# Performance work log

Hardware: AMD Instinct MI355X
Metric: run time of the kernel (lower is better)

## Reference

```python
import jax, jax.numpy as jnp
import numpy as np

NEG_SLOPE = 0.2       # PyG GATConv default leaky_relu negative_slope
NUM_GRAPHS = 128
VOCAB, HID, HEADS, NCLS = 5000, 64, 4, 20
N_NODES, N_EDGES = 50000, 1600000


def gat_conv(x, src, dst, W, a_src, a_dst, bias, concat):
    """PyG-style GATConv (eval mode, self-loops already in src/dst).
    W: [in, H*C]; a_src/a_dst: [H, C]; bias: [H*C] if concat else [C]."""
    N = x.shape[0]
    H, C = a_src.shape
    h = (x @ W).reshape(N, H, C)                      # [N,H,C]
    al_src = jnp.sum(h * a_src, axis=-1)              # [N,H]
    al_dst = jnp.sum(h * a_dst, axis=-1)              # [N,H]
    e = al_src[src] + al_dst[dst]                     # [E,H]
    e = jnp.where(e > 0, e, NEG_SLOPE * e)            # leaky_relu
    # segment softmax over incoming edges of each dst node
    emax = jax.lax.stop_gradient(jax.ops.segment_max(e, dst, num_segments=N))
    emax = jnp.where(jnp.isfinite(emax), emax, 0.0)
    ex = jnp.exp(e - emax[dst])
    denom = jax.ops.segment_sum(ex, dst, num_segments=N)
    alpha = ex / (denom[dst] + 1e-16)                 # [E,H]
    out = jax.ops.segment_sum(h[src] * alpha[..., None], dst, num_segments=N)  # [N,H,C]
    out = out.reshape(N, H * C) if concat else out.mean(axis=1)
    return out + bias


def setup_inputs() -> dict:
    key = jax.random.key(0)
    ks = jax.random.split(key, 12)
    C1 = HID // HEADS

    def xavier(k, shape):
        fan_in, fan_out = shape[0], shape[-1]
        lim = np.sqrt(6.0 / (fan_in + fan_out))
        return jax.random.uniform(k, shape, jnp.float32, -lim, lim)

    return {
        "x": jax.random.normal(ks[0], (N_NODES, VOCAB), jnp.float32),
        "edge_index": jax.random.randint(ks[1], (2, N_EDGES), 0, N_NODES, jnp.int32),
        "batch": jnp.sort(jax.random.randint(ks[2], (N_NODES,), 0, NUM_GRAPHS, jnp.int32)),
        "W1": xavier(ks[3], (VOCAB, HID)),
        "a_src1": xavier(ks[4], (HEADS, C1)),
        "a_dst1": xavier(ks[5], (HEADS, C1)),
        "b1": jnp.zeros((HID,), jnp.float32),
        "W2": xavier(ks[6], (HID, HID)),
        "a_src2": xavier(ks[7], (1, HID)),
        "a_dst2": xavier(ks[8], (1, HID)),
        "b2": jnp.zeros((HID,), jnp.float32),
        "Wc": xavier(ks[9], (HID, NCLS)),
        "bc": jnp.zeros((NCLS,), jnp.float32),
    }


def reference(x, edge_index, batch, W1, a_src1, a_dst1, b1,
              W2, a_src2, a_dst2, b2, Wc, bc):
    N = x.shape[0]
    loop = jnp.arange(N, dtype=edge_index.dtype)
    src = jnp.concatenate([edge_index[0], loop])      # add self-loops (PyG default)
    dst = jnp.concatenate([edge_index[1], loop])

    h = jax.nn.elu(gat_conv(x, src, dst, W1, a_src1, a_dst1, b1, concat=True))
    h = jax.nn.elu(gat_conv(h, src, dst, W2, a_src2, a_dst2, b2, concat=False))

    # global_mean_pool over batch ids
    sums = jax.ops.segment_sum(h, batch, num_segments=NUM_GRAPHS)           # [G,HID]
    cnts = jax.ops.segment_sum(jnp.ones((N, 1), h.dtype), batch, num_segments=NUM_GRAPHS)
    pooled = sums / jnp.maximum(cnts, 1.0)

    logits = pooled @ Wc + bc
    return jax.nn.log_softmax(logits, axis=1)
```

## Files before the change

### kernel.cpp

```cpp
#include <hip/hip_runtime.h>

#define N_NODES 50000
#define VOCAB   5000
#define KPAD1   5024
#define HID     64
#define HEADS   4
#define NCLS    20
#define NGRAPH  128
#define N_EDGES 1600000
#define ETOT    (N_EDGES + N_NODES)

typedef __attribute__((ext_vector_type(8))) short short8;
typedef __attribute__((ext_vector_type(4))) float f32x4;

__device__ inline ushort f2bf(float x) {
  union { float f; unsigned u; } c; c.f = x;
  unsigned r = (c.u + 0x7fffu + ((c.u >> 16) & 1u)) >> 16;
  return (ushort)r;
}

__global__ void cvtT_kernel(const float* __restrict__ W, ushort* __restrict__ Bt,
                            int K, int KP) {
  int i = blockIdx.x * blockDim.x + threadIdx.x;
  if (i >= 64 * KP) return;
  int n = i / KP, k = i - n * KP;
  Bt[i] = (k < K) ? f2bf(W[(size_t)k * 64 + n]) : (ushort)0;
}

template<int KT, int KP>
__global__ __launch_bounds__(256) void gemm_stream(const float* __restrict__ A,
    const ushort* __restrict__ Bt, float* __restrict__ D, int M) {
  int gt = blockIdx.x * 256 + threadIdx.x;
  int gw = gt >> 6, lane = gt & 63;
  int lr = lane & 15, quad = lane >> 4;
  int m0 = gw * 16;
  if (m0 >= M) return;
  const float*  ap = A  + (size_t)(m0 + lr) * KT + quad * 8;
  const ushort* bp = Bt + (size_t)lr * KP + quad * 8;
  f32x4 acc[4] = {{0,0,0,0},{0,0,0,0},{0,0,0,0},{0,0,0,0}};
  constexpr int KF = (KT / 32) * 32;
  #pragma unroll 2
  for (int k0 = 0; k0 < KF; k0 += 32) {
    float4 v0 = *(const float4*)(ap + k0);
    float4 v1 = *(const float4*)(ap + k0 + 4);
    short8 b0 = *(const short8*)(bp + k0);
    short8 b1 = *(const short8*)(bp + 16 * KP + k0);
    short8 b2 = *(const short8*)(bp + 32 * KP + k0);
    short8 b3 = *(const short8*)(bp + 48 * KP + k0);
    short8 af;
    af[0] = (short)f2bf(v0.x); af[1] = (short)f2bf(v0.y);
    af[2] = (short)f2bf(v0.z); af[3] = (short)f2bf(v0.w);
    af[4] = (short)f2bf(v1.x); af[5] = (short)f2bf(v1.y);
    af[6] = (short)f2bf(v1.z); af[7] = (short)f2bf(v1.w);
    acc[0] = __builtin_amdgcn_mfma_f32_16x16x32_bf16(af, b0, acc[0], 0, 0, 0);
    acc[1] = __builtin_amdgcn_mfma_f32_16x16x32_bf16(af, b1, acc[1], 0, 0, 0);
    acc[2] = __builtin_amdgcn_mfma_f32_16x16x32_bf16(af, b2, acc[2], 0, 0, 0);
    acc[3] = __builtin_amdgcn_mfma_f32_16x16x32_bf16(af, b3, acc[3], 0, 0, 0);
  }
  if (KT % 32) {
    int k0 = KF;
    float4 v0 = make_float4(0,0,0,0), v1 = make_float4(0,0,0,0);
    if (quad == 0) { v0 = *(const float4*)(ap + k0); v1 = *(const float4*)(ap + k0 + 4); }
    short8 b0 = *(const short8*)(bp + k0);
    short8 b1 = *(const short8*)(bp + 16 * KP + k0);
    short8 b2 = *(const short8*)(bp + 32 * KP + k0);
    short8 b3 = *(const short8*)(bp + 48 * KP + k0);
    short8 af;
    af[0] = (short)f2bf(v0.x); af[1] = (short)f2bf(v0.y);
    af[2] = (short)f2bf(v0.z); af[3] = (short)f2bf(v0.w);
    af[4] = (short)f2bf(v1.x); af[5] = (short)f2bf(v1.y);
    af[6] = (short)f2bf(v1.z); af[7] = (short)f2bf(v1.w);
    acc[0] = __builtin_amdgcn_mfma_f32_16x16x32_bf16(af, b0, acc[0], 0, 0, 0);
    acc[1] = __builtin_amdgcn_mfma_f32_16x16x32_bf16(af, b1, acc[1], 0, 0, 0);
    acc[2] = __builtin_amdgcn_mfma_f32_16x16x32_bf16(af, b2, acc[2], 0, 0, 0);
    acc[3] = __builtin_amdgcn_mfma_f32_16x16x32_bf16(af, b3, acc[3], 0, 0, 0);
  }
  #pragma unroll
  for (int ct = 0; ct < 4; ++ct)
    #pragma unroll
    for (int r = 0; r < 4; ++r)
      D[(size_t)(m0 + quad * 4 + r) * 64 + ct * 16 + lr] = acc[ct][r];
}

__global__ void al_h4_kernel(const float* __restrict__ h, const float* __restrict__ a_src,
                             const float* __restrict__ a_dst, float* __restrict__ alS,
                             float* __restrict__ alD, int n) {
  int wid = (blockIdx.x * blockDim.x + threadIdx.x) >> 6;
  int lane = threadIdx.x & 63;
  if (wid >= n) return;
  float hv = h[(size_t)wid * 64 + lane];
  float s = hv * a_src[lane];
  float d = hv * a_dst[lane];
  #pragma unroll
  for (int off = 1; off < 16; off <<= 1) {
    s += __shfl_down(s, off, 16);
    d += __shfl_down(d, off, 16);
  }
  if ((lane & 15) == 0) {
    alS[wid * 4 + (lane >> 4)] = s;
    alD[wid * 4 + (lane >> 4)] = d;
  }
}

__global__ void al_h1_kernel(const float* __restrict__ h, const float* __restrict__ a_src,
                             const float* __restrict__ a_dst, float* __restrict__ alS,
                             float* __restrict__ alD, int n) {
  int wid = (blockIdx.x * blockDim.x + threadIdx.x) >> 6;
  int lane = threadIdx.x & 63;
  if (wid >= n) return;
  float hv = h[(size_t)wid * 64 + lane];
  float s = hv * a_src[lane];
  float d = hv * a_dst[lane];
  #pragma unroll
  for (int off = 1; off < 64; off <<= 1) {
    s += __shfl_down(s, off, 64);
    d += __shfl_down(d, off, 64);
  }
  if (lane == 0) { alS[wid] = s; alD[wid] = d; }
}

__global__ void hist_kernel(const int* __restrict__ dstA, int* __restrict__ deg, int E, int Etot) {
  int i = blockIdx.x * blockDim.x + threadIdx.x;
  if (i >= Etot) return;
  int d = (i < E) ? dstA[i] : (i - E);
  atomicAdd(&deg[d], 1);
}

__global__ __launch_bounds__(1024) void scan_kernel(const int* __restrict__ deg,
                                                    int* __restrict__ indptr, int n) {
  __shared__ int wsum[16];
  __shared__ int carry;
  int t = threadIdx.x, w = t >> 6, lane = t & 63;
  if (t == 0) carry = 0;
  __syncthreads();
  for (int base = 0; base < n; base += 1024) {
    int i = base + t;
    int v = (i < n) ? deg[i] : 0;
    int x = v;
    #pragma unroll
    for (int off = 1; off < 64; off <<= 1) {
      int y = __shfl_up(x, off, 64);
      if (lane >= off) x += y;
    }
    if (lane == 63) wsum[w] = x;
    __syncthreads();
    if (w == 0 && lane < 16) {
      int y = wsum[lane];
      #pragma unroll
      for (int off = 1; off < 16; off <<= 1) {
        int z = __shfl_up(y, off, 16);
        if (lane >= off) y += z;
      }
      wsum[lane] = y;
    }
    __syncthreads();
    int incl = x + (w > 0 ? wsum[w - 1] : 0) + carry;
    if (i < n) indptr[i] = incl - v;
    __syncthreads();
    if (t == 1023) carry = incl;
    __syncthreads();
  }
  if (t == 0) indptr[n] = carry;
}

__global__ void scatter_kernel(const int* __restrict__ srcA, const int* __restrict__ dstA,
                               const int* __restrict__ indptr, int* __restrict__ fill,
                               int* __restrict__ srcs, int E, int Etot) {
  int i = blockIdx.x * blockDim.x + threadIdx.x;
  if (i >= Etot) return;
  int d, s;
  if (i < E) { d = dstA[i]; s = srcA[i]; } else { d = i - E; s = d; }
  int pos = indptr[d] + atomicAdd(&fill[d], 1);
  srcs[pos] = s;
}

template<int H>
__global__ __launch_bounds__(256) void agg_kernel(const float* __restrict__ h,
    const float* __restrict__ alS, const float* __restrict__ alD,
    const int* __restrict__ indptr, const int* __restrict__ srcs,
    const float* __restrict__ bias, float* __restrict__ out, int n) {
  int wid = (blockIdx.x * blockDim.x + threadIdx.x) >> 6;
  int lane = threadIdx.x & 63;
  if (wid >= n) return;
  constexpr int C = 64 / H;
  int head = lane / C;
  float ald = alD[wid * H + head];
  int j0 = indptr[wid], j1 = indptr[wid + 1];
  float m = -3.0e38f, ssum = 0.f, acc = 0.f;
  int p0 = srcs[j0], p1 = srcs[j0 + 1], p2 = srcs[j0 + 2], p3 = srcs[j0 + 3];
  for (int j = j0; j < j1; j += 4) {
    int rem = j1 - j;
    int s0 = p0;
    int s1 = (rem > 1) ? p1 : p0;
    int s2 = (rem > 2) ? p2 : p0;
    int s3 = (rem > 3) ? p3 : p0;
    int jn = j + 4;
    if (jn < j1) { p0 = srcs[jn]; p1 = srcs[jn + 1]; p2 = srcs[jn + 2]; p3 = srcs[jn + 3]; }
    float e0 = alS[s0 * H + head] + ald;
    float e1 = alS[s1 * H + head] + ald;
    float e2 = alS[s2 * H + head] + ald;
    float e3 = alS[s3 * H + head] + ald;
    float h0 = h[(size_t)s0 * 64 + lane];
    float h1 = h[(size_t)s1 * 64 + lane];
    float h2 = h[(size_t)s2 * 64 + lane];
    float h3 = h[(size_t)s3 * 64 + lane];
    e0 = e0 > 0.f ? e0 : 0.2f * e0;
    e1 = e1 > 0.f ? e1 : 0.2f * e1;
    e2 = e2 > 0.f ? e2 : 0.2f * e2;
    e3 = e3 > 0.f ? e3 : 0.2f * e3;
    e1 = (rem > 1) ? e1 : -3.0e38f;
    e2 = (rem > 2) ? e2 : -3.0e38f;
    e3 = (rem > 3) ? e3 : -3.0e38f;
    float cm = fmaxf(fmaxf(e0, e1), fmaxf(e2, e3));
    float mn = fmaxf(m, cm);
    float sc = __expf(m - mn);
    float q0 = __expf(e0 - mn), q1 = __expf(e1 - mn);
    float q2 = __expf(e2 - mn), q3 = __expf(e3 - mn);
    ssum = ssum * sc + q0 + q1 + q2 + q3;
    acc  = acc  * sc + q0 * h0 + q1 * h1 + q2 * h2 + q3 * h3;
    m = mn;
  }
  float o = acc / (ssum + 1e-16f) + bias[lane];
  o = o > 0.f ? o : __expf(o) - 1.f;
  out[(size_t)wid * 64 + lane] = o;
}

__global__ void cnt_kernel(const int* __restrict__ batch, int* __restrict__ cnts, int n) {
  int i = blockIdx.x * blockDim.x + threadIdx.x;
  if (i < n) atomicAdd(&cnts[batch[i]], 1);
}

__global__ void pool_kernel(const float* __restrict__ h, const int* __restrict__ batch,
                            float* __restrict__ pooled, int n) {
  int wid = (blockIdx.x * blockDim.x + threadIdx.x) >> 6;
  int lane = threadIdx.x & 63;
  int n0 = wid * 64;
  if (n0 >= n) return;
  int n1 = min(n0 + 64, n);
  int g = batch[min(n0 + lane, n - 1)];
  int gf = __shfl(g, 0), gl = __shfl(g, 63);
  if (gf == gl && n1 == n0 + 64) {
    float a = 0.f;
    #pragma unroll 8
    for (int i = n0; i < n1; ++i) a += h[(size_t)i * 64 + lane];
    atomicAdd(&pooled[gf * 64 + lane], a);
  } else {
    int g_cur = batch[n0];
    float a = 0.f;
    for (int i = n0; i < n1; ++i) {
      int gg = batch[i];
      if (gg != g_cur) {
        atomicAdd(&pooled[g_cur * 64 + lane], a);
        a = 0.f; g_cur = gg;
      }
      a += h[(size_t)i * 64 + lane];
    }
    atomicAdd(&pooled[g_cur * 64 + lane], a);
  }
}

__global__ __launch_bounds__(128) void cls_kernel(const float* __restrict__ pooled,
    const int* __restrict__ cnts, const float* __restrict__ Wc,
    const float* __restrict__ bc, float* __restrict__ out) {
  int g = threadIdx.x;
  if (g >= NGRAPH) return;
  float inv = 1.f / fmaxf((float)cnts[g], 1.f);
  float p[64];
  #pragma unroll
  for (int k = 0; k < 64; ++k) p[k] = pooled[g * 64 + k] * inv;
  float lg[NCLS];
  float mx = -3.0e38f;
  #pragma unroll
  for (int c = 0; c < NCLS; ++c) {
    float v = bc[c];
    for (int k = 0; k < 64; ++k) v += p[k] * Wc[k * NCLS + c];
    lg[c] = v;
    mx = fmaxf(mx, v);
  }
  float se = 0.f;
  #pragma unroll
  for (int c = 0; c < NCLS; ++c) se += expf(lg[c] - mx);
  float ls = logf(se);
  #pragma unroll
  for (int c = 0; c < NCLS; ++c) out[g * NCLS + c] = lg[c] - mx - ls;
}

extern "C" void kernel_launch(void* const* d_in, const int* in_sizes, int n_in,
                              void* d_out, int out_size, void* d_ws, size_t ws_size,
                              hipStream_t stream) {
  const float* x      = (const float*)d_in[0];
  const int*   ei     = (const int*)d_in[1];
  const int*   batch  = (const int*)d_in[2];
  const float* W1     = (const float*)d_in[3];
  const float* a_src1 = (const float*)d_in[4];
  const float* a_dst1 = (const float*)d_in[5];
  const float* b1     = (const float*)d_in[6];
  const float* W2     = (const float*)d_in[7];
  const float* a_src2 = (const float*)d_in[8];
  const float* a_dst2 = (const float*)d_in[9];
  const float* b2     = (const float*)d_in[10];
  const float* Wc     = (const float*)d_in[11];
  const float* bc     = (const float*)d_in[12];
  float* out = (float*)d_out;

  const int* srcA = ei;
  const int* dstA = ei + N_EDGES;

  char* ws = (char*)d_ws;
  size_t off = 0;
  auto alloc = [&](size_t bytes) -> void* {
    void* p = ws + off;
    off = (off + bytes + 255) & ~(size_t)255;
    return p;
  };
  float* bufA   = (float*)alloc((size_t)N_NODES * 64 * 4);
  float* bufB   = (float*)alloc((size_t)N_NODES * 64 * 4);
  float* alS1   = (float*)alloc((size_t)N_NODES * 4 * 4);
  float* alD1   = (float*)alloc((size_t)N_NODES * 4 * 4);
  float* alS2   = (float*)alloc((size_t)N_NODES * 4);
  float* alD2   = (float*)alloc((size_t)N_NODES * 4);
  ushort* w1t   = (ushort*)alloc((size_t)64 * KPAD1 * 2);
  ushort* w2t   = (ushort*)alloc((size_t)64 * 64 * 2);
  int* deg      = (int*)alloc((size_t)N_NODES * 4);
  int* fill     = (int*)alloc((size_t)N_NODES * 4);
  int* indptr   = (int*)alloc((size_t)(N_NODES + 1) * 4);
  int* srcs     = (int*)alloc((size_t)(ETOT + 16) * 4);
  float* pooled = (float*)alloc((size_t)NGRAPH * 64 * 4);
  int* cnts     = (int*)alloc((size_t)NGRAPH * 4);

  hipMemsetAsync(deg, 0, (size_t)N_NODES * 4, stream);
  hipMemsetAsync(fill, 0, (size_t)N_NODES * 4, stream);
  hipMemsetAsync(pooled, 0, (size_t)NGRAPH * 64 * 4, stream);
  hipMemsetAsync(cnts, 0, (size_t)NGRAPH * 4, stream);

  cvtT_kernel<<<(64 * KPAD1 + 255) / 256, 256, 0, stream>>>(W1, w1t, VOCAB, KPAD1);
  cvtT_kernel<<<(64 * 64 + 255) / 256, 256, 0, stream>>>(W2, w2t, 64, 64);

  int egrid = (ETOT + 255) / 256;
  hist_kernel<<<egrid, 256, 0, stream>>>(dstA, deg, N_EDGES, ETOT);
  scan_kernel<<<1, 1024, 0, stream>>>(deg, indptr, N_NODES);
  scatter_kernel<<<egrid, 256, 0, stream>>>(srcA, dstA, indptr, fill, srcs, N_EDGES, ETOT);

  int nwaveBlocks = (N_NODES * 64 + 255) / 256;
  int gemmBlocks = ((N_NODES + 15) / 16 + 3) / 4;

  gemm_stream<VOCAB, KPAD1><<<gemmBlocks, 256, 0, stream>>>(x, w1t, bufA, N_NODES);
  al_h4_kernel<<<nwaveBlocks, 256, 0, stream>>>(bufA, a_src1, a_dst1, alS1, alD1, N_NODES);
  agg_kernel<4><<<nwaveBlocks, 256, 0, stream>>>(bufA, alS1, alD1, indptr, srcs, b1, bufB, N_NODES);

  gemm_stream<64, 64><<<gemmBlocks, 256, 0, stream>>>(bufB, w2t, bufA, N_NODES);
  al_h1_kernel<<<nwaveBlocks, 256, 0, stream>>>(bufA, a_src2, a_dst2, alS2, alD2, N_NODES);
  agg_kernel<1><<<nwaveBlocks, 256, 0, stream>>>(bufA, alS2, alD2, indptr, srcs, b2, bufB, N_NODES);

  cnt_kernel<<<(N_NODES + 255) / 256, 256, 0, stream>>>(batch, cnts, N_NODES);
  pool_kernel<<<((N_NODES + 63) / 64 * 64 + 255) / 256, 256, 0, stream>>>(bufB, batch, pooled, N_NODES);
  cls_kernel<<<1, 128, 0, stream>>>(pooled, cnts, Wc, bc, out);
}
```

Baseline: 1.995 ms.

## Fuse attention logits into GEMMs, store features as bf16, parallelize scan

The attention-coefficient reductions now run in the GEMM epilogues, which removes the separate al_h4/al_h1 kernels and their re-reads of h. Intermediate node features are stored as bf16 to halve gather traffic in the edge aggregation. The single-block serial CSR scan becomes a three-kernel block scan, and the weight transpose uses an LDS tile. GEMM1 also switches to nontemporal loads for x and smaller 128-thread blocks. The trade-off is lower precision in the intermediate features and extra kernel launches for the scan.

Result: slower. 2.049 ms (+2.7%).

```diff
diff --git a/kernel.cpp b/kernel.cpp
--- a/kernel.cpp
+++ b/kernel.cpp
@@ -9,6 +9,7 @@
 #define NGRAPH  128
 #define N_EDGES 1600000
 #define ETOT    (N_EDGES + N_NODES)
+#define SCAN_BLKS ((N_NODES + 255) / 256)
 
 typedef __attribute__((ext_vector_type(8))) short short8;
 typedef __attribute__((ext_vector_type(4))) float f32x4;
@@ -18,105 +19,144 @@
   unsigned r = (c.u + 0x7fffu + ((c.u >> 16) & 1u)) >> 16;
   return (ushort)r;
 }
-
-__global__ void cvtT_kernel(const float* __restrict__ W, ushort* __restrict__ Bt,
-                            int K, int KP) {
-  int i = blockIdx.x * blockDim.x + threadIdx.x;
-  if (i >= 64 * KP) return;
-  int n = i / KP, k = i - n * KP;
-  Bt[i] = (k < K) ? f2bf(W[(size_t)k * 64 + n]) : (ushort)0;
-}
-
-template<int KT, int KP>
-__global__ __launch_bounds__(256) void gemm_stream(const float* __restrict__ A,
-    const ushort* __restrict__ Bt, float* __restrict__ D, int M) {
-  int gt = blockIdx.x * 256 + threadIdx.x;
+__device__ inline float bf2f(ushort u) {
+  union { unsigned u; float f; } c; c.u = (unsigned)u << 16;
+  return c.f;
+}
+
+__global__ __launch_bounds__(256) void cvtT_tile(const float* __restrict__ W,
+                                                 ushort* __restrict__ Bt, int K, int KP) {
+  __shared__ ushort tile[64][65];
+  int t = threadIdx.x;
+  int k0 = blockIdx.x * 64;
+  int n = t & 63;
+  for (int kk = t >> 6; kk < 64; kk += 4) {
+    int k = k0 + kk;
+    tile[n][kk] = (k < K) ? f2bf(W[(size_t)k * 64 + n]) : (ushort)0;
+  }
+  __syncthreads();
+  int kk = t & 63;
+  for (int nn = t >> 6; nn < 64; nn += 4) {
+    int k = k0 + kk;
+    if (k < KP) Bt[(size_t)nn * KP + k] = tile[nn][kk];
+  }
+}
+
+__global__ __launch_bounds__(128) void gemm1_kernel(const float* __restrict__ A,
+    const ushort* __restrict__ Bt, ushort* __restrict__ Dh,
+    float* __restrict__ alS, float* __restrict__ alD,
+    const float* __restrict__ a_src, const float* __restrict__ a_dst, int M) {
+  int gt = blockIdx.x * 128 + threadIdx.x;
   int gw = gt >> 6, lane = gt & 63;
   int lr = lane & 15, quad = lane >> 4;
   int m0 = gw * 16;
   if (m0 >= M) return;
-  const float*  ap = A  + (size_t)(m0 + lr) * KT + quad * 8;
-  const ushort* bp = Bt + (size_t)lr * KP + quad * 8;
+  const float*  ap = A  + (size_t)(m0 + lr) * VOCAB + quad * 8;
+  const ushort* bp = Bt + (size_t)lr * KPAD1 + quad * 8;
   f32x4 acc[4] = {{0,0,0,0},{0,0,0,0},{0,0,0,0},{0,0,0,0}};
-  constexpr int KF = (KT / 32) * 32;
+  constexpr int KF = (VOCAB / 32) * 32;
   #pragma unroll 2
   for (int k0 = 0; k0 < KF; k0 += 32) {
-    float4 v0 = *(const float4*)(ap + k0);
-    float4 v1 = *(const float4*)(ap + k0 + 4);
+    f32x4 v0 = __builtin_nontemporal_load((const f32x4*)(ap + k0));
+    f32x4 v1 = __builtin_nontemporal_load((const f32x4*)(ap + k0 + 4));
     short8 b0 = *(const short8*)(bp + k0);
-    short8 b1 = *(const short8*)(bp + 16 * KP + k0);
-    short8 b2 = *(const short8*)(bp + 32 * KP + k0);
-    short8 b3 = *(const short8*)(bp + 48 * KP + k0);
+    short8 b1 = *(const short8*)(bp + 16 * KPAD1 + k0);
+    short8 b2 = *(const short8*)(bp + 32 * KPAD1 + k0);
+    short8 b3 = *(const short8*)(bp + 48 * KPAD1 + k0);
     short8 af;
-    af[0] = (short)f2bf(v0.x); af[1] = (short)f2bf(v0.y);
-    af[2] = (short)f2bf(v0.z); af[3] = (short)f2bf(v0.w);
-    af[4] = (short)f2bf(v1.x); af[5] = (short)f2bf(v1.y);
-    af[6] = (short)f2bf(v1.z); af[7] = (short)f2bf(v1.w);
+    #pragma unroll
+    for (int j = 0; j < 4; ++j) { af[j] = (short)f2bf(v0[j]); af[4 + j] = (short)f2bf(v1[j]); }
     acc[0] = __builtin_amdgcn_mfma_f32_16x16x32_bf16(af, b0, acc[0], 0, 0, 0);
     acc[1] = __builtin_amdgcn_mfma_f32_16x16x32_bf16(af, b1, acc[1], 0, 0, 0);
     acc[2] = __builtin_amdgcn_mfma_f32_16x16x32_bf16(af, b2, acc[2], 0, 0, 0);
     acc[3] = __builtin_amdgcn_mfma_f32_16x16x32_bf16(af, b3, acc[3], 0, 0, 0);
   }
-  if (KT % 32) {
+  {
     int k0 = KF;
-    float4 v0 = make_float4(0,0,0,0), v1 = make_float4(0,0,0,0);
-    if (quad == 0) { v0 = *(const float4*)(ap + k0); v1 = *(const float4*)(ap + k0 + 4); }
+    f32x4 v0 = {0,0,0,0}, v1 = {0,0,0,0};
+    if (quad == 0) {
+      v0 = *(const f32x4*)(ap + k0);
+      v1 = *(const f32x4*)(ap + k0 + 4);
+    }
     short8 b0 = *(const short8*)(bp + k0);
-    short8 b1 = *(const short8*)(bp + 16 * KP + k0);
-    short8 b2 = *(const short8*)(bp + 32 * KP + k0);
-    short8 b3 = *(const short8*)(bp + 48 * KP + k0);
+    short8 b1 = *(const short8*)(bp + 16 * KPAD1 + k0);
+    short8 b2 = *(const short8*)(bp + 32 * KPAD1 + k0);
+    short8 b3 = *(const short8*)(bp + 48 * KPAD1 + k0);
     short8 af;
-    af[0] = (short)f2bf(v0.x); af[1] = (short)f2bf(v0.y);
-    af[2] = (short)f2bf(v0.z); af[3] = (short)f2bf(v0.w);
-    af[4] = (short)f2bf(v1.x); af[5] = (short)f2bf(v1.y);
-    af[6] = (short)f2bf(v1.z); af[7] = (short)f2bf(v1.w);
+    #pragma unroll
+    for (int j = 0; j < 4; ++j) { af[j] = (short)f2bf(v0[j]); af[4 + j] = (short)f2bf(v1[j]); }
     acc[0] = __builtin_amdgcn_mfma_f32_16x16x32_bf16(af, b0, acc[0], 0, 0, 0);
     acc[1] = __builtin_amdgcn_mfma_f32_16x16x32_bf16(af, b1, acc[1], 0, 0, 0);
     acc[2] = __builtin_amdgcn_mfma_f32_16x16x32_bf16(af, b2, acc[2], 0, 0, 0);
     acc[3] = __builtin_amdgcn_mfma_f32_16x16x32_bf16(af, b3, acc[3], 0, 0, 0);
   }
-  #pragma unroll
-  for (int ct = 0; ct < 4; ++ct)
+  float a0 = a_src[lane], d0 = a_dst[lane];
+  #pragma unroll
+  for (int ct = 0; ct < 4; ++ct) {
+    float av = __shfl(a0, ct * 16 + lr);
+    float dv = __shfl(d0, ct * 16 + lr);
     #pragma unroll
-    for (int r = 0; r < 4; ++r)
-      D[(size_t)(m0 + quad * 4 + r) * 64 + ct * 16 + lr] = acc[ct][r];
-}
-
-__global__ void al_h4_kernel(const float* __restrict__ h, const float* __restrict__ a_src,
-                             const float* __restrict__ a_dst, float* __restrict__ alS,
-                             float* __restrict__ alD, int n) {
-  int wid = (blockIdx.x * blockDim.x + threadIdx.x) >> 6;
-  int lane = threadIdx.x & 63;
-  if (wid >= n) return;
-  float hv = h[(size_t)wid * 64 + lane];
-  float s = hv * a_src[lane];
-  float d = hv * a_dst[lane];
-  #pragma unroll
-  for (int off = 1; off < 16; off <<= 1) {
-    s += __shfl_down(s, off, 16);
-    d += __shfl_down(d, off, 16);
-  }
-  if ((lane & 15) == 0) {
-    alS[wid * 4 + (lane >> 4)] = s;
-    alD[wid * 4 + (lane >> 4)] = d;
-  }
-}
-
-__global__ void al_h1_kernel(const float* __restrict__ h, const float* __restrict__ a_src,
-                             const float* __restrict__ a_dst, float* __restrict__ alS,
-                             float* __restrict__ alD, int n) {
-  int wid = (blockIdx.x * blockDim.x + threadIdx.x) >> 6;
-  int lane = threadIdx.x & 63;
-  if (wid >= n) return;
-  float hv = h[(size_t)wid * 64 + lane];
-  float s = hv * a_src[lane];
-  float d = hv * a_dst[lane];
-  #pragma unroll
-  for (int off = 1; off < 64; off <<= 1) {
-    s += __shfl_down(s, off, 64);
-    d += __shfl_down(d, off, 64);
-  }
-  if (lane == 0) { alS[wid] = s; alD[wid] = d; }
+    for (int r = 0; r < 4; ++r) {
+      int grow = m0 + quad * 4 + r;
+      Dh[(size_t)grow * 64 + ct * 16 + lr] = f2bf(acc[ct][r]);
+      float s = acc[ct][r] * av;
+      float d = acc[ct][r] * dv;
+      s += __shfl_xor(s, 1); d += __shfl_xor(d, 1);
+      s += __shfl_xor(s, 2); d += __shfl_xor(d, 2);
+      s += __shfl_xor(s, 4); d += __shfl_xor(d, 4);
+      s += __shfl_xor(s, 8); d += __shfl_xor(d, 8);
+      if (lr == r * 4 + ct) {
+        alS[(size_t)grow * 4 + ct] = s;
+        alD[(size_t)grow * 4 + ct] = d;
+      }
+    }
+  }
+}
+
+__global__ __launch_bounds__(128) void gemm2_kernel(const ushort* __restrict__ A,
+    const ushort* __restrict__ Bt, ushort* __restrict__ Dh,
+    float* __restrict__ alS, float* __restrict__ alD,
+    const float* __restrict__ a_src, const float* __restrict__ a_dst, int M) {
+  int gt = blockIdx.x * 128 + threadIdx.x;
+  int gw = gt >> 6, lane = gt & 63;
+  int lr = lane & 15, quad = lane >> 4;
+  int m0 = gw * 16;
+  if (m0 >= M) return;
+  const ushort* ap = A  + (size_t)(m0 + lr) * 64 + quad * 8;
+  const ushort* bp = Bt + (size_t)lr * 64 + quad * 8;
+  f32x4 acc[4] = {{0,0,0,0},{0,0,0,0},{0,0,0,0},{0,0,0,0}};
+  #pragma unroll
+  for (int k0 = 0; k0 < 64; k0 += 32) {
+    short8 af = *(const short8*)(ap + k0);
+    #pragma unroll
+    for (int ct = 0; ct < 4; ++ct) {
+      short8 b = *(const short8*)(bp + ct * 16 * 64 + k0);
+      acc[ct] = __builtin_amdgcn_mfma_f32_16x16x32_bf16(af, b, acc[ct], 0, 0, 0);
+    }
+  }
+  float a0 = a_src[lane], d0 = a_dst[lane];
+  float av[4], dv[4];
+  #pragma unroll
+  for (int ct = 0; ct < 4; ++ct) {
+    av[ct] = __shfl(a0, ct * 16 + lr);
+    dv[ct] = __shfl(d0, ct * 16 + lr);
+  }
+  #pragma unroll
+  for (int r = 0; r < 4; ++r) {
+    int grow = m0 + quad * 4 + r;
+    float s = 0.f, d = 0.f;
+    #pragma unroll
+    for (int ct = 0; ct < 4; ++ct) {
+      Dh[(size_t)grow * 64 + ct * 16 + lr] = f2bf(acc[ct][r]);
+      s += acc[ct][r] * av[ct];
+      d += acc[ct][r] * dv[ct];
+    }
+    s += __shfl_xor(s, 1); d += __shfl_xor(d, 1);
+    s += __shfl_xor(s, 2); d += __shfl_xor(d, 2);
+    s += __shfl_xor(s, 4); d += __shfl_xor(d, 4);
+    s += __shfl_xor(s, 8); d += __shfl_xor(d, 8);
+    if (lr == r) { alS[grow] = s; alD[grow] = d; }
+  }
 }
 
 __global__ void hist_kernel(const int* __restrict__ dstA, int* __restrict__ deg, int E, int Etot) {
@@ -126,41 +166,50 @@
   atomicAdd(&deg[d], 1);
 }
 
-__global__ __launch_bounds__(1024) void scan_kernel(const int* __restrict__ deg,
-                                                    int* __restrict__ indptr, int n) {
-  __shared__ int wsum[16];
-  __shared__ int carry;
-  int t = threadIdx.x, w = t >> 6, lane = t & 63;
-  if (t == 0) carry = 0;
+__global__ __launch_bounds__(256) void scan_blk(const int* __restrict__ deg,
+    int* __restrict__ excl, int* __restrict__ bsum, int n) {
+  __shared__ int ws[4];
+  int t = threadIdx.x, lane = t & 63, w = t >> 6;
+  int i = blockIdx.x * 256 + t;
+  int v = (i < n) ? deg[i] : 0;
+  int x = v;
+  #pragma unroll
+  for (int off = 1; off < 64; off <<= 1) {
+    int y = __shfl_up(x, off, 64);
+    if (lane >= off) x += y;
+  }
+  if (lane == 63) ws[w] = x;
   __syncthreads();
-  for (int base = 0; base < n; base += 1024) {
-    int i = base + t;
-    int v = (i < n) ? deg[i] : 0;
-    int x = v;
-    #pragma unroll
-    for (int off = 1; off < 64; off <<= 1) {
-      int y = __shfl_up(x, off, 64);
-      if (lane >= off) x += y;
-    }
-    if (lane == 63) wsum[w] = x;
-    __syncthreads();
-    if (w == 0 && lane < 16) {
-      int y = wsum[lane];
-      #pragma unroll
-      for (int off = 1; off < 16; off <<= 1) {
-        int z = __shfl_up(y, off, 16);
-        if (lane >= off) y += z;
-      }
-      wsum[lane] = y;
-    }
-    __syncthreads();
-    int incl = x + (w > 0 ? wsum[w - 1] : 0) + carry;
-    if (i < n) indptr[i] = incl - v;
-    __syncthreads();
-    if (t == 1023) carry = incl;
-    __syncthreads();
-  }
-  if (t == 0) indptr[n] = carry;
+  int add = 0;
+  for (int k = 0; k < w; ++k) add += ws[k];
+  x += add;
+  if (i < n) excl[i] = x - v;
+  if (t == 255) bsum[blockIdx.x] = x;
+}
+
+__global__ __launch_bounds__(256) void scan_top(const int* __restrict__ bsum,
+    int* __restrict__ boff, int* __restrict__ indptr, int nb, int n) {
+  __shared__ int ws[4];
+  int t = threadIdx.x, lane = t & 63, w = t >> 6;
+  int v = (t < nb) ? bsum[t] : 0;
+  int x = v;
+  #pragma unroll
+  for (int off = 1; off < 64; off <<= 1) {
+    int y = __shfl_up(x, off, 64);
+    if (lane >= off) x += y;
+  }
+  if (lane == 63) ws[w] = x;
+  __syncthreads();
+  int add = 0;
+  for (int k = 0; k < w; ++k) add += ws[k];
+  x += add;
+  boff[t] = x - v;
+  if (t == nb - 1) indptr[n] = x;
+}
+
+__global__ void scan_add(int* __restrict__ indptr, const int* __restrict__ boff, int n) {
+  int i = blockIdx.x * blockDim.x + threadIdx.x;
+  if (i < n) indptr[i] += boff[i >> 8];
 }
 
 __global__ void scatter_kernel(const int* __restrict__ srcA, const int* __restrict__ dstA,
@@ -174,11 +223,11 @@
   srcs[pos] = s;
 }
 
-template<int H>
-__global__ __launch_bounds__(256) void agg_kernel(const float* __restrict__ h,
+template<int H, typename OT>
+__global__ __launch_bounds__(256) void agg_kernel(const ushort* __restrict__ h,
     const float* __restrict__ alS, const float* __restrict__ alD,
     const int* __restrict__ indptr, const int* __restrict__ srcs,
-    const float* __restrict__ bias, float* __restrict__ out, int n) {
+    const float* __restrict__ bias, OT* __restrict__ out, int n) {
   int wid = (blockIdx.x * blockDim.x + threadIdx.x) >> 6;
   int lane = threadIdx.x & 63;
   if (wid >= n) return;
@@ -200,10 +249,10 @@
     float e1 = alS[s1 * H + head] + ald;
     float e2 = alS[s2 * H + head] + ald;
     float e3 = alS[s3 * H + head] + ald;
-    float h0 = h[(size_t)s0 * 64 + lane];
-    float h1 = h[(size_t)s1 * 64 + lane];
-    float h2 = h[(size_t)s2 * 64 + lane];
-    float h3 = h[(size_t)s3 * 64 + lane];
+    float h0 = bf2f(h[(size_t)s0 * 64 + lane]);
+    float h1 = bf2f(h[(size_t)s1 * 64 + lane]);
+    float h2 = bf2f(h[(size_t)s2 * 64 + lane]);
+    float h3 = bf2f(h[(size_t)s3 * 64 + lane]);
     e0 = e0 > 0.f ? e0 : 0.2f * e0;
     e1 = e1 > 0.f ? e1 : 0.2f * e1;
     e2 = e2 > 0.f ? e2 : 0.2f * e2;
@@ -222,7 +271,8 @@
   }
   float o = acc / (ssum + 1e-16f) + bias[lane];
   o = o > 0.f ? o : __expf(o) - 1.f;
-  out[(size_t)wid * 64 + lane] = o;
+  if constexpr (sizeof(OT) == 2) out[(size_t)wid * 64 + lane] = (OT)f2bf(o);
+  else                           out[(size_t)wid * 64 + lane] = o;
 }
 
 __global__ void cnt_kernel(const int* __restrict__ batch, int* __restrict__ cnts, int n) {
@@ -313,8 +363,10 @@
     off = (off + bytes + 255) & ~(size_t)255;
     return p;
   };
-  float* bufA   = (float*)alloc((size_t)N_NODES * 64 * 4);
-  float* bufB   = (float*)alloc((size_t)N_NODES * 64 * 4);
+  ushort* h1    = (ushort*)alloc((size_t)N_NODES * 64 * 2);
+  ushort* h1b   = (ushort*)alloc((size_t)N_NODES * 64 * 2);
+  ushort* h2    = (ushort*)alloc((size_t)N_NODES * 64 * 2);
+  float* hout   = (float*)alloc((size_t)N_NODES * 64 * 4);
   float* alS1   = (float*)alloc((size_t)N_NODES * 4 * 4);
   float* alD1   = (float*)alloc((size_t)N_NODES * 4 * 4);
   float* alS2   = (float*)alloc((size_t)N_NODES * 4);
@@ -325,6 +377,8 @@
   int* fill     = (int*)alloc((size_t)N_NODES * 4);
   int* indptr   = (int*)alloc((size_t)(N_NODES + 1) * 4);
   int* srcs     = (int*)alloc((size_t)(ETOT + 16) * 4);
+  int* bsum     = (int*)alloc(256 * 4);
+  int* boff     = (int*)alloc(256 * 4);
   float* pooled = (float*)alloc((size_t)NGRAPH * 64 * 4);
   int* cnts     = (int*)alloc((size_t)NGRAPH * 4);
 
@@ -333,26 +387,26 @@
   hipMemsetAsync(pooled, 0, (size_t)NGRAPH * 64 * 4, stream);
   hipMemsetAsync(cnts, 0, (size_t)NGRAPH * 4, stream);
 
-  cvtT_kernel<<<(64 * KPAD1 + 255) / 256, 256, 0, stream>>>(W1, w1t, VOCAB, KPAD1);
-  cvtT_kernel<<<(64 * 64 + 255) / 256, 256, 0, stream>>>(W2, w2t, 64, 64);
+  cvtT_tile<<<(KPAD1 + 63) / 64, 256, 0, stream>>>(W1, w1t, VOCAB, KPAD1);
+  cvtT_tile<<<1, 256, 0, stream>>>(W2, w2t, 64, 64);
 
   int egrid = (ETOT + 255) / 256;
   hist_kernel<<<egrid, 256, 0, stream>>>(dstA, deg, N_EDGES, ETOT);
-  scan_kernel<<<1, 1024, 0, stream>>>(deg, indptr, N_NODES);
+  scan_blk<<<SCAN_BLKS, 256, 0, stream>>>(deg, indptr, bsum, N_NODES);
+  scan_top<<<1, 256, 0, stream>>>(bsum, boff, indptr, SCAN_BLKS, N_NODES);
+  scan_add<<<SCAN_BLKS, 256, 0, stream>>>(indptr, boff, N_NODES);
   scatter_kernel<<<egrid, 256, 0, stream>>>(srcA, dstA, indptr, fill, srcs, N_EDGES, ETOT);
 
   int nwaveBlocks = (N_NODES * 64 + 255) / 256;
-  int gemmBlocks = ((N_NODES + 15) / 16 + 3) / 4;
-
-  gemm_stream<VOCAB, KPAD1><<<gemmBlocks, 256, 0, stream>>>(x, w1t, bufA, N_NODES);
-  al_h4_kernel<<<nwaveBlocks, 256, 0, stream>>>(bufA, a_src1, a_dst1, alS1, alD1, N_NODES);
-  agg_kernel<4><<<nwaveBlocks, 256, 0, stream>>>(bufA, alS1, alD1, indptr, srcs, b1, bufB, N_NODES);
-
-  gemm_stream<64, 64><<<gemmBlocks, 256, 0, stream>>>(bufB, w2t, bufA, N_NODES);
-  al_h1_kernel<<<nwaveBlocks, 256, 0, stream>>>(bufA, a_src2, a_dst2, alS2, alD2, N_NODES);
-  agg_kernel<1><<<nwaveBlocks, 256, 0, stream>>>(bufA, alS2, alD2, indptr, srcs, b2, bufB, N_NODES);
+  int gemmBlocks = ((N_NODES + 15) / 16 + 1) / 2;
+
+  gemm1_kernel<<<gemmBlocks, 128, 0, stream>>>(x, w1t, h1, alS1, alD1, a_src1, a_dst1, N_NODES);
+  agg_kernel<4, ushort><<<nwaveBlocks, 256, 0, stream>>>(h1, alS1, alD1, indptr, srcs, b1, h1b, N_NODES);
+
+  gemm2_kernel<<<gemmBlocks, 128, 0, stream>>>(h1b, w2t, h2, alS2, alD2, a_src2, a_dst2, N_NODES);
+  agg_kernel<1, float><<<nwaveBlocks, 256, 0, stream>>>(h2, alS2, alD2, indptr, srcs, b2, hout, N_NODES);
 
   cnt_kernel<<<(N_NODES + 255) / 256, 256, 0, stream>>>(batch, cnts, N_NODES);
-  pool_kernel<<<((N_NODES + 63) / 64 * 64 + 255) / 256, 256, 0, stream>>>(bufB, batch, pooled, N_NODES);
+  pool_kernel<<<((N_NODES + 63) / 64 * 64 + 255) / 256, 256, 0, stream>>>(hout, batch, pooled, N_NODES);
   cls_kernel<<<1, 128, 0, stream>>>(pooled, cnts, Wc, bc, out);
 }
```
